# Optimization experiments

Hardware: AMD Instinct MI355X
Metric: run time of the kernel (lower is better)

## Reference

```python
import jax, jax.numpy as jnp
import numpy as np

N_NODES = 2048
N_EDGES = 32768
N_GRAPH = 64
D_INJ = 240
D_EMB = 480
D_FEAT = 512
H = 4
DH = 120
SH_DIM = 9
N_RBF = 128
CUTOFF = 5.0
AVG_DEGREE = 16.0
AVG_NUM_NODES = 32.0
N_ITER = 2
MAX_ATOM = 64


def _ln(x):
    mu = jnp.mean(x, axis=-1, keepdims=True)
    var = jnp.var(x, axis=-1, keepdims=True)
    return (x - mu) * jax.lax.rsqrt(var + 1e-6)


def _sph(u):
    # component-normalized real spherical harmonics l=0,1,2 of unit vectors u [E,3]
    x, y, z = u[:, 0], u[:, 1], u[:, 2]
    s3 = np.sqrt(3.0); s15 = np.sqrt(15.0); s5 = np.sqrt(5.0)
    return jnp.stack([
        jnp.ones_like(x),
        s3 * x, s3 * y, s3 * z,
        s15 * x * y, s15 * y * z,
        0.5 * s5 * (3.0 * z * z - 1.0),
        s15 * x * z, 0.5 * s15 * (x * x - y * y)], axis=-1)


def _block(z, esrc, edst, sh, rbf, Wq, Wk, Wv, Wsh, Wr, Wo, F1, F2, res_ffn):
    # equivariant-style dot-product attention: gather -> edge compute -> segment softmax -> scatter
    x = _ln(z)
    q = (x @ Wq)[edst].reshape(-1, H, DH)
    k = (x @ Wk)[esrc].reshape(-1, H, DH)
    v = (x @ Wv)[esrc].reshape(-1, H, DH)
    m = (sh @ Wsh).reshape(-1, H, DH)          # SH tensor-product message modulation
    r = jax.nn.silu(rbf @ Wr)[:, :, None]      # radial gate per head [E,H,1]
    k = (k + m) * r
    v = (v + m) * r
    logit = jnp.sum(q * k, axis=-1) / np.sqrt(DH)   # [E,H]
    mx = jax.ops.segment_max(logit, edst, num_segments=N_NODES)
    mx = jnp.where(jnp.isfinite(mx), mx, 0.0)
    ex = jnp.exp(logit - mx[edst])
    den = jax.ops.segment_sum(ex, edst, num_segments=N_NODES)
    alpha = ex / (den[edst] + 1e-9)
    agg = jax.ops.segment_sum(alpha[:, :, None] * v, edst, num_segments=N_NODES)
    y = z + agg.reshape(N_NODES, H * DH) @ Wo
    out = jax.nn.silu(_ln(y) @ F1) @ F2
    return y + out if res_ffn else out


def _forward(pos, atom_table, degWr, degWsh,
             b0_Wq, b0_Wk, b0_Wv, b0_Wsh, b0_Wr, b0_Wo, b0_F1, b0_F2,
             bm_Wq, bm_Wk, bm_Wv, bm_Wsh, bm_Wr, bm_Wo, bm_F1, bm_F2,
             bf_Wq, bf_Wk, bf_Wv, bf_Wsh, bf_Wr, bf_Wo, bf_F1, bf_F2,
             hW1, hW2, node_atom, edge_src, edge_dst, batch):
    # ---- encode ----
    vec = pos[edge_src] - pos[edge_dst]
    d = jnp.sqrt(jnp.sum(vec * vec, axis=-1) + 1e-12)
    sh = _sph(vec / d[:, None])                              # [E,9]
    centers = jnp.linspace(0.0, CUTOFF, N_RBF)
    width = CUTOFF / N_RBF
    rbf = jnp.exp(-0.5 * jnp.square((d[:, None] - centers) / width))  # [E,128]
    atom = atom_table[node_atom]                             # [N,240]
    rad = jax.nn.silu(rbf @ degWr)                           # [E,9]
    deg = jax.ops.segment_sum((sh * rad) @ degWsh, edge_dst, num_segments=N_NODES) / AVG_DEGREE
    inj = atom + deg                                         # input-injection features
    # ---- DEQ fixed-point (unrolled) ----
    z = jnp.zeros((N_NODES, D_EMB), dtype=pos.dtype)
    for _ in range(N_ITER):
        z = _block(jnp.concatenate([z, inj], axis=-1), edge_src, edge_dst, sh, rbf,
                   b0_Wq, b0_Wk, b0_Wv, b0_Wsh, b0_Wr, b0_Wo, b0_F1, b0_F2, False)
        for i in range(4):
            z = _block(z, edge_src, edge_dst, sh, rbf,
                       bm_Wq[i], bm_Wk[i], bm_Wv[i], bm_Wsh[i], bm_Wr[i],
                       bm_Wo[i], bm_F1[i], bm_F2[i], True)
    # ---- decode ----
    feat = _block(z, edge_src, edge_dst, sh, rbf,
                  bf_Wq, bf_Wk, bf_Wv, bf_Wsh, bf_Wr, bf_Wo, bf_F1, bf_F2, False)
    feat = _ln(feat)
    e_node = jax.nn.silu(feat @ hW1) @ hW2                   # [N,1]
    return jax.ops.segment_sum(e_node, batch, num_segments=N_GRAPH) / np.sqrt(AVG_NUM_NODES)


def setup_inputs() -> dict:
    key = jax.random.key(0)
    it = iter(jax.random.split(key, 40))
    def nrm(shape):
        fan = shape[-2] if len(shape) >= 2 else shape[-1]
        return jax.random.normal(next(it), shape, jnp.float32) / np.sqrt(fan)
    inp = {}
    inp['pos'] = jax.random.normal(next(it), (N_NODES, 3), jnp.float32) * 2.0
    inp['node_atom'] = jax.random.randint(next(it), (N_NODES,), 0, MAX_ATOM)
    inp['edge_src'] = jax.random.randint(next(it), (N_EDGES,), 0, N_NODES)
    inp['edge_dst'] = jax.random.randint(next(it), (N_EDGES,), 0, N_NODES)
    inp['batch'] = jnp.sort(jax.random.randint(next(it), (N_NODES,), 0, N_GRAPH))
    inp['atom_table'] = nrm((MAX_ATOM, D_INJ))
    inp['degWr'] = nrm((N_RBF, SH_DIM))
    inp['degWsh'] = nrm((SH_DIM, D_INJ))
    DZ = D_EMB + D_INJ
    inp['b0_Wq'] = nrm((DZ, H * DH)); inp['b0_Wk'] = nrm((DZ, H * DH)); inp['b0_Wv'] = nrm((DZ, H * DH))
    inp['b0_Wsh'] = nrm((SH_DIM, H * DH)); inp['b0_Wr'] = nrm((N_RBF, H))
    inp['b0_Wo'] = nrm((H * DH, DZ)); inp['b0_F1'] = nrm((DZ, D_EMB)); inp['b0_F2'] = nrm((D_EMB, D_EMB))
    inp['bm_Wq'] = nrm((4, D_EMB, H * DH)); inp['bm_Wk'] = nrm((4, D_EMB, H * DH)); inp['bm_Wv'] = nrm((4, D_EMB, H * DH))
    inp['bm_Wsh'] = nrm((4, SH_DIM, H * DH)); inp['bm_Wr'] = nrm((4, N_RBF, H))
    inp['bm_Wo'] = nrm((4, H * DH, D_EMB)); inp['bm_F1'] = nrm((4, D_EMB, D_EMB)); inp['bm_F2'] = nrm((4, D_EMB, D_EMB))
    inp['bf_Wq'] = nrm((D_EMB, H * DH)); inp['bf_Wk'] = nrm((D_EMB, H * DH)); inp['bf_Wv'] = nrm((D_EMB, H * DH))
    inp['bf_Wsh'] = nrm((SH_DIM, H * DH)); inp['bf_Wr'] = nrm((N_RBF, H))
    inp['bf_Wo'] = nrm((H * DH, D_EMB)); inp['bf_F1'] = nrm((D_EMB, D_EMB)); inp['bf_F2'] = nrm((D_EMB, D_FEAT))
    inp['hW1'] = nrm((D_FEAT, D_FEAT)); inp['hW2'] = nrm((D_FEAT, 1))
    return inp


def reference(pos, atom_table, degWr, degWsh,
              b0_Wq, b0_Wk, b0_Wv, b0_Wsh, b0_Wr, b0_Wo, b0_F1, b0_F2,
              bm_Wq, bm_Wk, bm_Wv, bm_Wsh, bm_Wr, bm_Wo, bm_F1, bm_F2,
              bf_Wq, bf_Wk, bf_Wv, bf_Wsh, bf_Wr, bf_Wo, bf_F1, bf_F2,
              hW1, hW2, node_atom, edge_src, edge_dst, batch):
    return _forward(pos, atom_table, degWr, degWsh,
                    b0_Wq, b0_Wk, b0_Wv, b0_Wsh, b0_Wr, b0_Wo, b0_F1, b0_F2,
                    bm_Wq, bm_Wk, bm_Wv, bm_Wsh, bm_Wr, bm_Wo, bm_F1, bm_F2,
                    bf_Wq, bf_Wk, bf_Wv, bf_Wsh, bf_Wr, bf_Wo, bf_F1, bf_F2,
                    hW1, hW2, node_atom, edge_src, edge_dst, batch)
```

## Files before the change

### kernel.cpp

```cpp
#include <hip/hip_runtime.h>

#define NN 2048
#define NE 32768
#define NG 64
#define DINJ 240
#define DEMB 480
#define DFEAT 512
#define MAXDEG 192

typedef unsigned short ushort_t;
typedef __attribute__((ext_vector_type(8))) short short8;
typedef __attribute__((ext_vector_type(4))) float floatx4;

__device__ __forceinline__ float b2f(ushort_t u){
  union { unsigned u; float f; } x; x.u = ((unsigned)u) << 16; return x.f;
}
__device__ __forceinline__ ushort_t f2b(float f){
  union { float f; unsigned u; } x; x.f = f;
  unsigned r = x.u + 0x7FFFu + ((x.u >> 16) & 1u);
  return (ushort_t)(r >> 16);
}
__device__ __forceinline__ float wredsum(float v){
  #pragma unroll
  for (int o = 32; o > 0; o >>= 1) v += __shfl_xor(v, o, 64);
  return v;
}
__device__ __forceinline__ float silu_f(float x){ return x / (1.f + __expf(-x)); }

__global__ void zero_f32(float* p, int n){
  int i = blockIdx.x*256 + threadIdx.x; if (i < n) p[i] = 0.f;
}

__global__ void detect_kernel(const ushort_t* __restrict__ probe, int* flag){
  __shared__ int c;
  if (threadIdx.x == 0) c = 0;
  __syncthreads();
  ushort_t u = probe[2*threadIdx.x];
  int e = (u >> 7) & 0xFF;
  int plausible = (u == 0) || (e >= 100 && e <= 140);
  atomicAdd(&c, plausible);
  __syncthreads();
  if (threadIdx.x == 0) *flag = (c >= 192) ? 0 : 1;
}

struct CDesc { const void* src; float* dst; int n; };
struct CDescArr { CDesc d[11]; };
__global__ __launch_bounds__(256) void convert_inputs(CDescArr ca, const int* __restrict__ flag){
  CDesc cd = ca.d[blockIdx.y];
  int isf32 = *flag;
  for (int i = blockIdx.x*256 + threadIdx.x; i < cd.n; i += gridDim.x*256){
    cd.dst[i] = isf32 ? ((const float*)cd.src)[i] : b2f(((const ushort_t*)cd.src)[i]);
  }
}

struct TDesc { const void* src; ushort_t* dh; ushort_t* dl; int K; int M; int Kpad; int Mpad; int eoff; };
struct TDescArr { TDesc d[37]; };
__global__ __launch_bounds__(256) void transpose_all(TDescArr ta, const int* __restrict__ flag){
  TDesc td = ta.d[blockIdx.z];
  int k0 = blockIdx.x*32, m0 = blockIdx.y*32;
  if (k0 >= td.Kpad || m0 >= td.Mpad) return;
  int isf32 = *flag;
  __shared__ float lds[32*33];
  int tx = threadIdx.x & 31, ty = threadIdx.x >> 5;
  #pragma unroll
  for (int r = 0; r < 4; ++r){
    int kl = ty + r*8;
    int k = k0 + kl, mm = m0 + tx;
    float x = 0.f;
    if (k < td.K && mm < td.M){
// ... 51 lines not shown
  sh[4] = s15*ix*iy; sh[5] = s15*iy*iz; sh[6] = 0.5f*s5*(3.f*iz*iz - 1.f);
  sh[7] = s15*ix*iz; sh[8] = 0.5f*s15*(ix*ix - iy*iy);
  #pragma unroll
  for (int j = 0; j < 9; ++j) sh_out[(size_t)e*9+j] = sh[j];
  float t9a[9], ga[24];
  #pragma unroll
  for (int j = 0; j < 9; ++j) t9a[j] = 0.f;
  #pragma unroll
  for (int o = 0; o < 24; ++o) ga[o] = 0.f;
  for (int k = 0; k < 128; ++k){
    float c = (float)k * (5.0f/127.0f);
    float u = (dd - c) * (128.0f/5.0f);
    float rb = __expf(-0.5f*u*u);
    const float* w9  = w9L + k*9;
    const float* w24 = w24L + k*24;
    #pragma unroll
    for (int j = 0; j < 9; ++j) t9a[j] += rb*w9[j];
    #pragma unroll
    for (int o = 0; o < 24; ++o) ga[o] += rb*w24[o];
  }
  #pragma unroll
  for (int j = 0; j < 9; ++j) t9[(size_t)e*9+j] = sh[j]*silu_f(t9a[j]);
  #pragma unroll
  for (int o = 0; o < 24; ++o){
    int slot = o >> 2, h = o & 3;
    r_all[((size_t)slot*NE + e)*4 + h] = silu_f(ga[o]);
  }
}

__global__ void hist_kernel(const int* __restrict__ edst, int* counts){
  int e = blockIdx.x*256 + threadIdx.x; if (e < NE) atomicAdd(&counts[edst[e]], 1);
}
__global__ __launch_bounds__(1024) void scan_kernel(const int* __restrict__ counts,
                                                    int* rowptr, int* cursor){
  __shared__ int s[1024];
  int t = threadIdx.x;
  int c0 = counts[2*t], c1 = counts[2*t+1];
  s[t] = c0 + c1;
  __syncthreads();
  for (int off = 1; off < 1024; off <<= 1){
    int v = (t >= off) ? s[t-off] : 0;
    __syncthreads();
    s[t] += v;
    __syncthreads();
  }
  int excl = s[t] - (c0 + c1);
  rowptr[2*t]   = excl;       cursor[2*t]   = excl;
  rowptr[2*t+1] = excl + c0;  cursor[2*t+1] = excl + c0;
  if (t == 1023) rowptr[2048] = s[1023];
}
__global__ void scatter_kernel(const int* __restrict__ edst, int* cursor, int* perm){
  int e = blockIdx.x*256 + threadIdx.x; if (e >= NE) return;
  int p = atomicAdd(&cursor[edst[e]], 1);
  perm[p] = e;
}

__global__ __launch_bounds__(64) void inj_kernel(const float* __restrict__ t9,
    const int* __restrict__ rowptr, const int* __restrict__ perm,
    const int* __restrict__ node_atom, const float* __restrict__ atom_table,
    const float* __restrict__ degWsh, float* __restrict__ inj){
  int i = blockIdx.x; int lane = threadIdx.x;
  int b = rowptr[i], e = rowptr[i+1];
  float T[9];
  #pragma unroll
  for (int j = 0; j < 9; ++j) T[j] = 0.f;
  for (int idx = b; idx < e; ++idx){
    int ed = perm[idx];
    #pragma unroll
    for (int j = 0; j < 9; ++j) T[j] += t9[(size_t)ed*9+j];
  }
  int a = node_atom[i];
  for (int c = lane; c < DINJ; c += 64){
    float s = 0.f;
    #pragma unroll
    for (int j = 0; j < 9; ++j) s += T[j]*degWsh[j*DINJ+c];
    inj[(size_t)i*DINJ+c] = atom_table[(size_t)a*DINJ+c] + s*(1.0f/16.0f);
  }
}

__global__ __launch_bounds__(256) void ln_kernel(const float* __restrict__ in, int D,
                                                 int Kpad, ushort_t* __restrict__ oh){
  int i = blockIdx.x*4 + (threadIdx.x >> 6);
  int lane = threadIdx.x & 63;
  const float* row = in + (size_t)i*D;
  float s = 0.f, sq = 0.f;
  for (int d = lane; d < D; d += 64){ float x = row[d]; s += x; sq += x*x; }
  s = wredsum(s); sq = wredsum(sq);
  float mu = s / (float)D;
  float var = fmaxf(sq / (float)D - mu*mu, 0.f);
  float rs = rsqrtf(var + 1e-6f);
  ushort_t* ohrow = oh + (size_t)i*Kpad;
  for (int d = lane; d < D; d += 64) ohrow[d] = f2b((row[d]-mu)*rs);
  for (int d = D + lane; d < Kpad; d += 64) ohrow[d] = 0;
}

__global__ __launch_bounds__(256) void ln_cat_kernel(const float* __restrict__ z,
    const float* __restrict__ inj, ushort_t* __restrict__ oh){
  int i = blockIdx.x*4 + (threadIdx.x >> 6);
  int lane = threadIdx.x & 63;
  const float* zr = z + (size_t)i*480;
  const float* ir = inj + (size_t)i*240;
  float s = 0.f, sq = 0.f;
  for (int d = lane; d < 720; d += 64){
    float x = (d < 480) ? zr[d] : ir[d-480];
    s += x; sq += x*x;
  }
  s = wredsum(s); sq = wredsum(sq);
  float mu = s * (1.0f/720.0f);
  float var = fmaxf(sq * (1.0f/720.0f) - mu*mu, 0.f);
  float rs = rsqrtf(var + 1e-6f);
  ushort_t* ohrow = oh + (size_t)i*736;
  for (int d = lane; d < 720; d += 64){
    float x = (d < 480) ? zr[d] : ir[d-480];
    ohrow[d] = f2b((x-mu)*rs);
  }
  for (int d = 720 + lane; d < 736; d += 64) ohrow[d] = 0;
}

template<int KPAD, bool SPLITB>
__global__ __launch_bounds__(256) void gemm_bt(
    const ushort_t* __restrict__ A,
    const ushort_t* __restrict__ BTh, const ushort_t* __restrict__ BTl,
    int N, int ldc,
    float* __restrict__ Cf, ushort_t* __restrict__ Cb,
    const float* __restrict__ R, const float* __restrict__ R2, int flags){
  int lane = threadIdx.x & 63, wave = threadIdx.x >> 6;
  int row0 = blockIdx.y*64 + (wave>>1)*32;
  int col0 = blockIdx.x*64 + (wave&1)*32;
  int m = lane & 15, q4 = lane >> 4;
  size_t a0 = (size_t)(row0+m)*KPAD + q4*8;
  size_t a1 = a0 + (size_t)16*KPAD;
  size_t b0 = (size_t)(col0+m)*KPAD + q4*8;
  size_t b1 = b0 + (size_t)16*KPAD;
  floatx4 acc00 = {0,0,0,0}, acc01 = {0,0,0,0}, acc10 = {0,0,0,0}, acc11 = {0,0,0,0};
  constexpr int steps = KPAD >> 5;
  constexpr int DEPTH = SPLITB ? 3 : 4;
  struct Frag { short8 A0, A1, B0h, B1h, B0l, B1l; };
  auto loadF = [&](int s) -> Frag {
    Frag f;
    size_t o = (size_t)s*32;
    f.A0  = *(const short8*)(A   + a0 + o);
    f.A1  = *(const short8*)(A   + a1 + o);
    f.B0h = *(const short8*)(BTh + b0 + o);
    f.B1h = *(const short8*)(BTh + b1 + o);
    if (SPLITB){
      f.B0l = *(const short8*)(BTl + b0 + o);
      f.B1l = *(const short8*)(BTl + b1 + o);
    }
    return f;
  };
  Frag ring[DEPTH];
  #pragma unroll
  for (int d = 0; d < DEPTH; ++d) ring[d] = loadF(d < steps ? d : steps-1);
  #pragma unroll
  for (int s = 0; s < steps; ++s){
    Frag cur = ring[s % DEPTH];
    if (s + DEPTH < steps) ring[s % DEPTH] = loadF(s + DEPTH);
    acc00 = __builtin_amdgcn_mfma_f32_16x16x32_bf16(cur.A0, cur.B0h, acc00, 0, 0, 0);
    acc01 = __builtin_amdgcn_mfma_f32_16x16x32_bf16(cur.A0, cur.B1h, acc01, 0, 0, 0);
    acc10 = __builtin_amdgcn_mfma_f32_16x16x32_bf16(cur.A1, cur.B0h, acc10, 0, 0, 0);
    acc11 = __builtin_amdgcn_mfma_f32_16x16x32_bf16(cur.A1, cur.B1h, acc11, 0, 0, 0);
    if (SPLITB){
      acc00 = __builtin_amdgcn_mfma_f32_16x16x32_bf16(cur.A0, cur.B0l, acc00, 0, 0, 0);
      acc01 = __builtin_amdgcn_mfma_f32_16x16x32_bf16(cur.A0, cur.B1l, acc01, 0, 0, 0);
      acc10 = __builtin_amdgcn_mfma_f32_16x16x32_bf16(cur.A1, cur.B0l, acc10, 0, 0, 0);
      acc11 = __builtin_amdgcn_mfma_f32_16x16x32_bf16(cur.A1, cur.B1l, acc11, 0, 0, 0);
    }
  }
  #pragma unroll
  for (int rr = 0; rr < 2; ++rr){
    #pragma unroll
    for (int cc = 0; cc < 2; ++cc){
      int col = col0 + cc*16 + m;
      if (col >= N) continue;
      floatx4 acc = rr ? (cc ? acc11 : acc10) : (cc ? acc01 : acc00);
      int rowb = row0 + rr*16 + q4*4;
      #pragma unroll
      for (int r = 0; r < 4; ++r){
        int row = rowb + r;
        float v = acc[r];
        if (flags & 16){
          if (col < 960) Cf[(size_t)row*960 + col] = v;
          else           Cb[(size_t)row*480 + (col - 960)] = f2b(v);
          continue;
        }
        size_t idx = (size_t)row*ldc + col;
        if (flags & 2){
          if (flags & 8)
            v += (col < 480) ? R[(size_t)row*480 + col] : R2[(size_t)row*240 + (col-480)];
          else
            v += R[idx];
        }
        if (flags & 1) v = silu_f(v);
        if (flags & 4) Cb[idx] = f2b(v);
        else           Cf[idx] = v;
      }
    }
  }
}

__global__ __launch_bounds__(256) void node_attn_kernel(
    const float* __restrict__ qk, const ushort_t* __restrict__ vb,
    const float* __restrict__ sh,
    const float* __restrict__ Wsh, const float* __restrict__ r_slot,
    const int* __restrict__ rowptr, const int* __restrict__ perm,
    const int* __restrict__ esrc, ushort_t* __restrict__ aggh){
  int i = blockIdx.x; int t = threadIdx.x;
  int lane = t & 63, w = t >> 6;
  int b = rowptr[i]; int deg = min(rowptr[i+1] - b, MAXDEG);
  __shared__ float qL[480];
  __shared__ float PqL[36];
  __shared__ float logitL[MAXDEG*4];
  __shared__ float rL[MAXDEG*4];
  __shared__ int eL[MAXDEG], srcL[MAXDEG];
  __shared__ float S[36];
  __shared__ float mxs[4], dens[4];
  for (int d = t; d < 480; d += 256) qL[d] = qk[(size_t)i*960 + d];
  for (int idx = t; idx < deg; idx += 256){
    int e = perm[b+idx];
    eL[idx] = e;
    srcL[idx] = esrc[e];
  }
  __syncthreads();
  if (t < 144){
    int o = t >> 2;
// ... 125 lines not shown
  const void* bm_Wsh = d_in[19];
  const void* bm_Wr  = d_in[20];
  const void* bm_Wo  = d_in[21];
  const void* bm_F1  = d_in[22];
  const void* bm_F2  = d_in[23];
  const void* bf_Wq  = d_in[24];
  const void* bf_Wk  = d_in[25];
  const void* bf_Wv  = d_in[26];
  const void* bf_Wsh = d_in[27];
  const void* bf_Wr  = d_in[28];
  const void* bf_Wo  = d_in[29];
  const void* bf_F1  = d_in[30];
  const void* bf_F2  = d_in[31];
  const void* hW1    = d_in[32];
  const void* hW2    = d_in[33];

  char* bws = (char*)d_ws;
  size_t off = 0;
  auto alloc = [&](size_t bytes) -> void* {
    void* p = bws + off;
    off += (bytes + 255) & ~(size_t)255;
    return p;
  };
  int* dflag   = (int*)alloc(256);
  float* sh_f  = (float*)alloc((size_t)NE*9*4);
  float* t9    = (float*)alloc((size_t)NE*9*4);
  int* counts  = (int*)alloc(2048*4);
  int* rowptr  = (int*)alloc(2049*4);
  int* cursor  = (int*)alloc(2048*4);
  int* perm    = (int*)alloc((size_t)NE*4);
  float* injb  = (float*)alloc((size_t)NN*DINJ*4);
  float* zA    = (float*)alloc((size_t)NN*512*4);
  float* zB    = (float*)alloc((size_t)NN*512*4);
  ushort_t* xlnh = (ushort_t*)alloc((size_t)NN*736*2);
  float* qkf   = (float*)alloc((size_t)NN*960*4);
  ushort_t* vbuf = (ushort_t*)alloc((size_t)NN*480*2);
  float* Wr_all = (float*)alloc((size_t)128*24*4);
  float* r_all = (float*)alloc((size_t)6*NE*4*4);
  ushort_t* aggh = (ushort_t*)alloc((size_t)NN*DEMB*2);
  float* ybuf  = (float*)alloc((size_t)NN*720*4);
  ushort_t* h1h = (ushort_t*)alloc((size_t)NN*DEMB*2);
  ushort_t* g1h = (ushort_t*)alloc((size_t)NN*DFEAT*2);
  float* gsum  = (float*)alloc(64*4);

  float* pos_c    = (float*)alloc((size_t)NN*3*4);
  float* atom_c   = (float*)alloc((size_t)64*DINJ*4);
  float* degWr_c  = (float*)alloc((size_t)128*9*4);
  float* degWsh_c = (float*)alloc((size_t)9*DINJ*4);
  float* b0_Wsh_c = (float*)alloc((size_t)9*480*4);
  float* b0_Wr_c  = (float*)alloc((size_t)128*4*4);
  float* bm_Wsh_c = (float*)alloc((size_t)4*9*480*4);
  float* bm_Wr_c  = (float*)alloc((size_t)4*128*4*4);
  float* bf_Wsh_c = (float*)alloc((size_t)9*480*4);
  float* bf_Wr_c  = (float*)alloc((size_t)128*4*4);
  float* hW2_c    = (float*)alloc((size_t)512*4);

  auto allocW = [&](size_t elems, ushort_t*& h, ushort_t*& l){
    h = (ushort_t*)alloc(elems*2); l = (ushort_t*)alloc(elems*2);
  };
  ushort_t *b0_qkvTh,*b0_qkvTl,*b0_WoTh,*b0_WoTl,*b0_F1Th,*b0_F1Tl,*b0_F2Th,*b0_F2Tl;
  allocW((size_t)1472*736, b0_qkvTh, b0_qkvTl);
  allocW((size_t)768*480,  b0_WoTh,  b0_WoTl);
  allocW((size_t)512*736,  b0_F1Th,  b0_F1Tl);
  allocW((size_t)512*480,  b0_F2Th,  b0_F2Tl);
  ushort_t *bm_qkvTh[4],*bm_qkvTl[4],*bm_WoTh[4],*bm_WoTl[4],*bm_F1Th[4],*bm_F1Tl[4],*bm_F2Th[4],*bm_F2Tl[4];
  for (int i = 0; i < 4; ++i){
    allocW((size_t)1472*480, bm_qkvTh[i], bm_qkvTl[i]);
    allocW((size_t)512*480,  bm_WoTh[i],  bm_WoTl[i]);
    allocW((size_t)512*480,  bm_F1Th[i],  bm_F1Tl[i]);
    allocW((size_t)512*480,  bm_F2Th[i],  bm_F2Tl[i]);
  }
  ushort_t *bf_qkvTh,*bf_qkvTl,*bf_WoTh,*bf_WoTl,*bf_F1Th,*bf_F1Tl,*bf_F2Th,*bf_F2Tl,*hW1Th,*hW1Tl;
  allocW((size_t)1472*480, bf_qkvTh, bf_qkvTl);
  allocW((size_t)512*480,  bf_WoTh,  bf_WoTl);
  allocW((size_t)512*480,  bf_F1Th,  bf_F1Tl);
  allocW((size_t)512*480,  bf_F2Th,  bf_F2Tl);
  allocW((size_t)512*512,  hW1Th,    hW1Tl);

  detect_kernel<<<1, 256, 0, stream>>>((const ushort_t*)atom_table, dflag);

  CDescArr ca;
  int ci = 0;
  auto addC = [&](const void* s, float* d, int n){
    ca.d[ci].src = s; ca.d[ci].dst = d; ca.d[ci].n = n; ++ci;
  };
  addC(pos, pos_c, NN*3);
  addC(atom_table, atom_c, 64*DINJ);
  addC(degWr, degWr_c, 128*9);
  addC(degWsh, degWsh_c, 9*DINJ);
  addC(b0_Wsh, b0_Wsh_c, 9*480);
  addC(b0_Wr, b0_Wr_c, 128*4);
  addC(bm_Wsh, bm_Wsh_c, 4*9*480);
  addC(bm_Wr, bm_Wr_c, 4*128*4);
  addC(bf_Wsh, bf_Wsh_c, 9*480);
  addC(bf_Wr, bf_Wr_c, 128*4);
  addC(hW2, hW2_c, 512);
  convert_inputs<<<dim3(8, 11), 256, 0, stream>>>(ca, dflag);

  TDescArr ta;
  int ti = 0;
  auto addT = [&](const void* s, ushort_t* dh, ushort_t* dl, int K, int M,
                  int Kp, int Mp, int rowoff, int eo){
    ta.d[ti].src = s;
    ta.d[ti].dh = dh + (size_t)rowoff*Kp;
    ta.d[ti].dl = dl + (size_t)rowoff*Kp;
    ta.d[ti].K = K; ta.d[ti].M = M; ta.d[ti].Kpad = Kp; ta.d[ti].Mpad = Mp;
    ta.d[ti].eoff = eo; ++ti;
  };
  addT(b0_Wq, b0_qkvTh, b0_qkvTl, 720, 480, 736, 480, 0,   0);
  addT(b0_Wk, b0_qkvTh, b0_qkvTl, 720, 480, 736, 480, 480, 0);
  addT(b0_Wv, b0_qkvTh, b0_qkvTl, 720, 480, 736, 512, 960, 0);
  addT(b0_Wo, b0_WoTh,  b0_WoTl,  480, 720, 480, 768, 0,   0);
  addT(b0_F1, b0_F1Th,  b0_F1Tl,  720, 480, 736, 512, 0,   0);
  addT(b0_F2, b0_F2Th,  b0_F2Tl,  480, 480, 480, 512, 0,   0);
  for (int i = 0; i < 4; ++i){
    int eo = i*480*480;
    addT(bm_Wq, bm_qkvTh[i], bm_qkvTl[i], 480, 480, 480, 480, 0,   eo);
    addT(bm_Wk, bm_qkvTh[i], bm_qkvTl[i], 480, 480, 480, 480, 480, eo);
    addT(bm_Wv, bm_qkvTh[i], bm_qkvTl[i], 480, 480, 480, 512, 960, eo);
    addT(bm_Wo, bm_WoTh[i],  bm_WoTl[i],  480, 480, 480, 512, 0,   eo);
    addT(bm_F1, bm_F1Th[i],  bm_F1Tl[i],  480, 480, 480, 512, 0,   eo);
    addT(bm_F2, bm_F2Th[i],  bm_F2Tl[i],  480, 480, 480, 512, 0,   eo);
  }
  addT(bf_Wq, bf_qkvTh, bf_qkvTl, 480, 480, 480, 480, 0,   0);
  addT(bf_Wk, bf_qkvTh, bf_qkvTl, 480, 480, 480, 480, 480, 0);
  addT(bf_Wv, bf_qkvTh, bf_qkvTl, 480, 480, 480, 512, 960, 0);
  addT(bf_Wo, bf_WoTh,  bf_WoTl,  480, 480, 480, 512, 0,   0);
  addT(bf_F1, bf_F1Th,  bf_F1Tl,  480, 480, 480, 512, 0,   0);
  addT(bf_F2, bf_F2Th,  bf_F2Tl,  480, 512, 480, 512, 0,   0);
  addT(hW1,   hW1Th,    hW1Tl,    512, 512, 512, 512, 0,   0);
  transpose_all<<<dim3(23, 24, 37), 256, 0, stream>>>(ta, dflag);

  pack_wr<<<12, 256, 0, stream>>>(b0_Wr_c, bm_Wr_c, bf_Wr_c, Wr_all);
  edge_all_kernel<<<NE/128, 128, 0, stream>>>(pos_c, esrc, edst, degWr_c, Wr_all,
                                              sh_f, t9, r_all);

  zero_f32<<<(2048 + 255)/256, 256, 0, stream>>>((float*)counts, 2048);
  hist_kernel<<<NE/256, 256, 0, stream>>>(edst, counts);
  scan_kernel<<<1, 1024, 0, stream>>>(counts, rowptr, cursor);
  scatter_kernel<<<NE/256, 256, 0, stream>>>(edst, cursor, perm);

  inj_kernel<<<NN, 64, 0, stream>>>(t9, rowptr, perm, node_atom, atom_c, degWsh_c, injb);
  zero_f32<<<(NN*DEMB)/256, 256, 0, stream>>>(zA, NN*DEMB);

  auto gemm = [&](const ushort_t* A, const ushort_t* BTh, const ushort_t* BTl,
                  int N, int Npad, int Kp, int ldc,
                  float* Cf, ushort_t* Cb, const float* R, const float* R2,
                  int flags, bool split){
    dim3 g(Npad/64, 32);
    if (split){
      if (Kp == 480)
        gemm_bt<480,true><<<g, 256, 0, stream>>>(A, BTh, BTl, N, ldc, Cf, Cb, R, R2, flags);
      else if (Kp == 512)
        gemm_bt<512,true><<<g, 256, 0, stream>>>(A, BTh, BTl, N, ldc, Cf, Cb, R, R2, flags);
      else
        gemm_bt<736,true><<<g, 256, 0, stream>>>(A, BTh, BTl, N, ldc, Cf, Cb, R, R2, flags);
    } else {
      if (Kp == 480)
        gemm_bt<480,false><<<g, 256, 0, stream>>>(A, BTh, BTl, N, ldc, Cf, Cb, R, R2, flags);
      else if (Kp == 512)
        gemm_bt<512,false><<<g, 256, 0, stream>>>(A, BTh, BTl, N, ldc, Cf, Cb, R, R2, flags);
      else
        gemm_bt<736,false><<<g, 256, 0, stream>>>(A, BTh, BTl, N, ldc, Cf, Cb, R, R2, flags);
    }
  };

  struct BW {
    const float *Wsh, *r_slot;
    const ushort_t *qkvTh,*qkvTl,*WoTh,*WoTl,*F1Th,*F1Tl,*F2Th,*F2Tl;
    int Din, Kpad, Dout; bool res;
  };
  auto run_block = [&](const BW& bw, const float* zin, const float* zinj, float* zout){
    if (zinj) ln_cat_kernel<<<NN/4, 256, 0, stream>>>(zin, zinj, xlnh);
    else      ln_kernel<<<NN/4, 256, 0, stream>>>(zin, bw.Din, bw.Kpad, xlnh);
    gemm(xlnh, bw.qkvTh, bw.qkvTl, 1440, 1472, bw.Kpad, 960,
         qkf, vbuf, nullptr, nullptr, 16, true);
    node_attn_kernel<<<NN, 256, 0, stream>>>(qkf, vbuf, sh_f, bw.Wsh, bw.r_slot,
                                             rowptr, perm, esrc, aggh);
    int WoNpad = (bw.Din == 720) ? 768 : 512;
    gemm(aggh, bw.WoTh, bw.WoTl, bw.Din, WoNpad, 480, bw.Din,
         ybuf, nullptr, zin, zinj, zinj ? (2|8) : 2, false);
    ln_kernel<<<NN/4, 256, 0, stream>>>(ybuf, bw.Din, bw.Kpad, xlnh);
    gemm(xlnh, bw.F1Th, bw.F1Tl, DEMB, 512, bw.Kpad, DEMB,
         nullptr, h1h, nullptr, nullptr, 1|4, false);
    gemm(h1h, bw.F2Th, bw.F2Tl, bw.Dout, 512, 480, bw.Dout,
         zout, nullptr, bw.res ? ybuf : nullptr, nullptr, bw.res ? 2 : 0, false);
  };

  BW b0 = { b0_Wsh_c, r_all + (size_t)0*NE*4,
            b0_qkvTh,b0_qkvTl,b0_WoTh,b0_WoTl,b0_F1Th,b0_F1Tl,b0_F2Th,b0_F2Tl,
            720, 736, 480, false };
  BW bm[4];
  for (int i = 0; i < 4; ++i){
    bm[i] = { bm_Wsh_c + (size_t)i*9*480, r_all + (size_t)(1+i)*NE*4,
              bm_qkvTh[i],bm_qkvTl[i],bm_WoTh[i],bm_WoTl[i],
              bm_F1Th[i],bm_F1Tl[i],bm_F2Th[i],bm_F2Tl[i],
              480, 480, 480, true };
  }
  BW bf = { bf_Wsh_c, r_all + (size_t)5*NE*4,
            bf_qkvTh,bf_qkvTl,bf_WoTh,bf_WoTl,bf_F1Th,bf_F1Tl,bf_F2Th,bf_F2Tl,
            480, 480, 512, false };

  float* z  = zA;
  float* z2 = zB;
  for (int iter = 0; iter < 2; ++iter){
    run_block(b0, z, injb, z2);
    { float* tmp = z; z = z2; z2 = tmp; }
    for (int i = 0; i < 4; ++i){
      run_block(bm[i], z, nullptr, z2);
      { float* tmp = z; z = z2; z2 = tmp; }
    }
  }
  run_block(bf, z, nullptr, z2);
  ln_kernel<<<NN/4, 256, 0, stream>>>(z2, DFEAT, DFEAT, xlnh);
  gemm(xlnh, hW1Th, hW1Tl, DFEAT, 512, DFEAT, DFEAT,
       nullptr, g1h, nullptr, nullptr, 1|4, true);
  zero_f32<<<1, 64, 0, stream>>>(gsum, 64);
  head_dot_kernel<<<NN/4, 256, 0, stream>>>(g1h, hW2_c, batch, gsum);
  finalize_kernel<<<1, 64, 0, stream>>>(gsum, dflag, d_out);
}
```

Measured before the change: 1.362 ms.

## Fuse LayerNorm into consumer GEMMs using row statistics from producer epilogues

Producer kernels (inj_kernel and the Wo and F2 GEMM epilogues) now write per-row partial sums and sums of squares into slot buffers. A new gemm_ln kernel adds up these partials to get each row's mean and rstd. It then normalizes and converts the fp32 A operand to bf16 as it loads it, so the standalone ln/ln_cat kernels and the bf16 xlnh buffer are gone. This cuts kernel launches and one full activation round-trip per LayerNorm. In exchange, A is read as fp32 and normalized again in every column block, most heavily in the wide QKV GEMM.

```diff
diff --git a/kernel.cpp b/kernel.cpp
--- a/kernel.cpp
+++ b/kernel.cpp
@@ -178,7 +178,8 @@
 __global__ __launch_bounds__(64) void inj_kernel(const float* __restrict__ t9,
     const int* __restrict__ rowptr, const int* __restrict__ perm,
     const int* __restrict__ node_atom, const float* __restrict__ atom_table,
-    const float* __restrict__ degWsh, float* __restrict__ inj){
+    const float* __restrict__ degWsh, float* __restrict__ inj,
+    float* __restrict__ statInj){
   int i = blockIdx.x; int lane = threadIdx.x;
   int b = rowptr[i], e = rowptr[i+1];
   float T[9];
@@ -190,51 +191,17 @@
     for (int j = 0; j < 9; ++j) T[j] += t9[(size_t)ed*9+j];
   }
   int a = node_atom[i];
+  float ss = 0.f, sq = 0.f;
   for (int c = lane; c < DINJ; c += 64){
     float s = 0.f;
     #pragma unroll
     for (int j = 0; j < 9; ++j) s += T[j]*degWsh[j*DINJ+c];
-    inj[(size_t)i*DINJ+c] = atom_table[(size_t)a*DINJ+c] + s*(1.0f/16.0f);
-  }
-}
-
-__global__ __launch_bounds__(256) void ln_kernel(const float* __restrict__ in, int D,
-                                                 int Kpad, ushort_t* __restrict__ oh){
-  int i = blockIdx.x*4 + (threadIdx.x >> 6);
-  int lane = threadIdx.x & 63;
-  const float* row = in + (size_t)i*D;
-  float s = 0.f, sq = 0.f;
-  for (int d = lane; d < D; d += 64){ float x = row[d]; s += x; sq += x*x; }
-  s = wredsum(s); sq = wredsum(sq);
-  float mu = s / (float)D;
-  float var = fmaxf(sq / (float)D - mu*mu, 0.f);
-  float rs = rsqrtf(var + 1e-6f);
-  ushort_t* ohrow = oh + (size_t)i*Kpad;
-  for (int d = lane; d < D; d += 64) ohrow[d] = f2b((row[d]-mu)*rs);
-  for (int d = D + lane; d < Kpad; d += 64) ohrow[d] = 0;
-}
-
-__global__ __launch_bounds__(256) void ln_cat_kernel(const float* __restrict__ z,
-    const float* __restrict__ inj, ushort_t* __restrict__ oh){
-  int i = blockIdx.x*4 + (threadIdx.x >> 6);
-  int lane = threadIdx.x & 63;
-  const float* zr = z + (size_t)i*480;
-  const float* ir = inj + (size_t)i*240;
-  float s = 0.f, sq = 0.f;
-  for (int d = lane; d < 720; d += 64){
-    float x = (d < 480) ? zr[d] : ir[d-480];
-    s += x; sq += x*x;
-  }
-  s = wredsum(s); sq = wredsum(sq);
-  float mu = s * (1.0f/720.0f);
-  float var = fmaxf(sq * (1.0f/720.0f) - mu*mu, 0.f);
-  float rs = rsqrtf(var + 1e-6f);
-  ushort_t* ohrow = oh + (size_t)i*736;
-  for (int d = lane; d < 720; d += 64){
-    float x = (d < 480) ? zr[d] : ir[d-480];
-    ohrow[d] = f2b((x-mu)*rs);
-  }
-  for (int d = 720 + lane; d < 736; d += 64) ohrow[d] = 0;
+    float val = atom_table[(size_t)a*DINJ+c] + s*(1.0f/16.0f);
+    inj[(size_t)i*DINJ+c] = val;
+    ss += val; sq += val*val;
+  }
+  ss = wredsum(ss); sq = wredsum(sq);
+  if (lane == 0){ statInj[i*2] = ss; statInj[i*2+1] = sq; }
 }
 
 template<int KPAD, bool SPLITB>
@@ -243,7 +210,8 @@
     const ushort_t* __restrict__ BTh, const ushort_t* __restrict__ BTl,
     int N, int ldc,
     float* __restrict__ Cf, ushort_t* __restrict__ Cb,
-    const float* __restrict__ R, const float* __restrict__ R2, int flags){
+    const float* __restrict__ R, const float* __restrict__ R2, int flags,
+    float* __restrict__ statOut){
   int lane = threadIdx.x & 63, wave = threadIdx.x >> 6;
   int row0 = blockIdx.y*64 + (wave>>1)*32;
   int col0 = blockIdx.x*64 + (wave&1)*32;
@@ -287,6 +255,153 @@
       acc11 = __builtin_amdgcn_mfma_f32_16x16x32_bf16(cur.A1, cur.B1l, acc11, 0, 0, 0);
     }
   }
+  float srow[2][4] = {{0,0,0,0},{0,0,0,0}};
+  float qrow[2][4] = {{0,0,0,0},{0,0,0,0}};
+  #pragma unroll
+  for (int rr = 0; rr < 2; ++rr){
+    #pragma unroll
+    for (int cc = 0; cc < 2; ++cc){
+      int col = col0 + cc*16 + m;
+      if (col >= N) continue;
+      floatx4 acc = rr ? (cc ? acc11 : acc10) : (cc ? acc01 : acc00);
+      int rowb = row0 + rr*16 + q4*4;
+      #pragma unroll
+      for (int r = 0; r < 4; ++r){
+        int row = rowb + r;
+        float v = acc[r];
+        size_t idx = (size_t)row*ldc + col;
+        if (flags & 2){
+          if (flags & 8)
+            v += (col < 480) ? R[(size_t)row*480 + col] : R2[(size_t)row*240 + (col-480)];
+          else
+            v += R[idx];
+        }
+        if (flags & 1) v = silu_f(v);
+        if (statOut){ srow[rr][r] += v; qrow[rr][r] += v*v; }
+        if (flags & 4) Cb[idx] = f2b(v);
+        else           Cf[idx] = v;
+      }
+    }
+  }
+  if (statOut){
+    int slot = blockIdx.x*2 + (wave&1);
+    #pragma unroll
+    for (int rr = 0; rr < 2; ++rr){
+      #pragma unroll
+      for (int r = 0; r < 4; ++r){
+        float s = srow[rr][r], q = qrow[rr][r];
+        #pragma unroll
+        for (int o = 1; o < 16; o <<= 1){
+          s += __shfl_xor(s, o, 64);
+          q += __shfl_xor(q, o, 64);
+        }
+        if (m == 0){
+          int row = row0 + rr*16 + q4*4 + r;
+          float* p = statOut + ((size_t)slot*NN + row)*2;
+          p[0] = s; p[1] = q;
+        }
+      }
+    }
+  }
+}
+
+template<int KPAD, bool SPLITB>
+__global__ __launch_bounds__(256) void gemm_ln(
+    const float* __restrict__ Az, const float* __restrict__ Ainj,
+    int L1, int L2,
+    const float* __restrict__ statA, const float* __restrict__ statInj, int nslot,
+    const ushort_t* __restrict__ BTh, const ushort_t* __restrict__ BTl,
+    int N, int ldc,
+    float* __restrict__ Cf, ushort_t* __restrict__ Cb, int flags){
+  __shared__ float muL[64], rsL[64];
+  int lane = threadIdx.x & 63, wave = threadIdx.x >> 6;
+  int row0b = blockIdx.y*64;
+  int t = threadIdx.x;
+  if (t < 64){
+    int row = row0b + t;
+    float s = 0.f, sq = 0.f;
+    for (int sl = 0; sl < nslot; ++sl){
+      const float* p = statA + ((size_t)sl*NN + row)*2;
+      s += p[0]; sq += p[1];
+    }
+    if (statInj){ s += statInj[row*2]; sq += statInj[row*2+1]; }
+    float D = (float)(L1 + L2);
+    float mu = s / D;
+    float var = fmaxf(sq / D - mu*mu, 0.f);
+    muL[t] = mu;
+    rsL[t] = rsqrtf(var + 1e-6f);
+  }
+  __syncthreads();
+  int row0 = row0b + (wave>>1)*32;
+  int col0 = blockIdx.x*64 + (wave&1)*32;
+  int m = lane & 15, q4 = lane >> 4;
+  int ra = (wave>>1)*32 + m;
+  float mu0 = muL[ra],    rs0 = rsL[ra];
+  float mu1 = muL[ra+16], rs1 = rsL[ra+16];
+  const float* pz0 = Az + (size_t)(row0 + m)*L1;
+  const float* pz1 = Az + (size_t)(row0 + 16 + m)*L1;
+  const float* pi0 = Ainj ? Ainj + (size_t)(row0 + m)*L2 : nullptr;
+  const float* pi1 = Ainj ? Ainj + (size_t)(row0 + 16 + m)*L2 : nullptr;
+  size_t b0 = (size_t)(col0+m)*KPAD + q4*8;
+  size_t b1 = b0 + (size_t)16*KPAD;
+  floatx4 acc00 = {0,0,0,0}, acc01 = {0,0,0,0}, acc10 = {0,0,0,0}, acc11 = {0,0,0,0};
+  constexpr int steps = KPAD >> 5;
+  constexpr int DEPTH = SPLITB ? 3 : 4;
+  int DD = L1 + L2;
+  auto loadA = [&](const float* pz, const float* pi, float mu, float rs, int k) -> short8 {
+    short8 r;
+    if (k + 8 <= L1){
+      float4 x0 = *(const float4*)(pz + k);
+      float4 x1 = *(const float4*)(pz + k + 4);
+      float v[8] = {x0.x,x0.y,x0.z,x0.w,x1.x,x1.y,x1.z,x1.w};
+      #pragma unroll
+      for (int j = 0; j < 8; ++j) r[j] = (short)f2b((v[j]-mu)*rs);
+    } else if (k < DD){
+      int kk = k - L1;
+      float4 x0 = *(const float4*)(pi + kk);
+      float4 x1 = *(const float4*)(pi + kk + 4);
+      float v[8] = {x0.x,x0.y,x0.z,x0.w,x1.x,x1.y,x1.z,x1.w};
+      #pragma unroll
+      for (int j = 0; j < 8; ++j) r[j] = (short)f2b((v[j]-mu)*rs);
+    } else {
+      #pragma unroll
+      for (int j = 0; j < 8; ++j) r[j] = 0;
+    }
+    return r;
+  };
+  struct Frag { short8 A0, A1, B0h, B1h, B0l, B1l; };
+  auto loadF = [&](int s) -> Frag {
+    Frag f;
+    int k = q4*8 + s*32;
+    f.A0 = loadA(pz0, pi0, mu0, rs0, k);
+    f.A1 = loadA(pz1, pi1, mu1, rs1, k);
+    size_t o = (size_t)s*32;
+    f.B0h = *(const short8*)(BTh + b0 + o);
+    f.B1h = *(const short8*)(BTh + b1 + o);
+    if (SPLITB){
+      f.B0l = *(const short8*)(BTl + b0 + o);
+      f.B1l = *(const short8*)(BTl + b1 + o);
+    }
+    return f;
+  };
+  Frag ring[DEPTH];
+  #pragma unroll
+  for (int d = 0; d < DEPTH; ++d) ring[d] = loadF(d < steps ? d : steps-1);
+  #pragma unroll
+  for (int s = 0; s < steps; ++s){
+    Frag cur = ring[s % DEPTH];
+    if (s + DEPTH < steps) ring[s % DEPTH] = loadF(s + DEPTH);
+    acc00 = __builtin_amdgcn_mfma_f32_16x16x32_bf16(cur.A0, cur.B0h, acc00, 0, 0, 0);
+    acc01 = __builtin_amdgcn_mfma_f32_16x16x32_bf16(cur.A0, cur.B1h, acc01, 0, 0, 0);
+    acc10 = __builtin_amdgcn_mfma_f32_16x16x32_bf16(cur.A1, cur.B0h, acc10, 0, 0, 0);
+    acc11 = __builtin_amdgcn_mfma_f32_16x16x32_bf16(cur.A1, cur.B1h, acc11, 0, 0, 0);
+    if (SPLITB){
+      acc00 = __builtin_amdgcn_mfma_f32_16x16x32_bf16(cur.A0, cur.B0l, acc00, 0, 0, 0);
+      acc01 = __builtin_amdgcn_mfma_f32_16x16x32_bf16(cur.A0, cur.B1l, acc01, 0, 0, 0);
+      acc10 = __builtin_amdgcn_mfma_f32_16x16x32_bf16(cur.A1, cur.B0l, acc10, 0, 0, 0);
+      acc11 = __builtin_amdgcn_mfma_f32_16x16x32_bf16(cur.A1, cur.B1l, acc11, 0, 0, 0);
+    }
+  }
   #pragma unroll
   for (int rr = 0; rr < 2; ++rr){
     #pragma unroll
@@ -305,12 +420,6 @@
           continue;
         }
         size_t idx = (size_t)row*ldc + col;
-        if (flags & 2){
-          if (flags & 8)
-            v += (col < 480) ? R[(size_t)row*480 + col] : R2[(size_t)row*240 + (col-480)];
-          else
-            v += R[idx];
-        }
         if (flags & 1) v = silu_f(v);
         if (flags & 4) Cb[idx] = f2b(v);
         else           Cf[idx] = v;
@@ -502,7 +611,6 @@
   float* injb  = (float*)alloc((size_t)NN*DINJ*4);
   float* zA    = (float*)alloc((size_t)NN*512*4);
   float* zB    = (float*)alloc((size_t)NN*512*4);
-  ushort_t* xlnh = (ushort_t*)alloc((size_t)NN*736*2);
   float* qkf   = (float*)alloc((size_t)NN*960*4);
   ushort_t* vbuf = (ushort_t*)alloc((size_t)NN*480*2);
   float* Wr_all = (float*)alloc((size_t)128*24*4);
@@ -512,6 +620,9 @@
   ushort_t* h1h = (ushort_t*)alloc((size_t)NN*DEMB*2);
   ushort_t* g1h = (ushort_t*)alloc((size_t)NN*DFEAT*2);
   float* gsum  = (float*)alloc(64*4);
+  float* statY   = (float*)alloc((size_t)24*NN*2*4);
+  float* statZ   = (float*)alloc((size_t)16*NN*2*4);
+  float* statInj = (float*)alloc((size_t)NN*2*4);
 
   float* pos_c    = (float*)alloc((size_t)NN*3*4);
   float* atom_c   = (float*)alloc((size_t)64*DINJ*4);
@@ -610,28 +721,53 @@
   scan_kernel<<<1, 1024, 0, stream>>>(counts, rowptr, cursor);
   scatter_kernel<<<NE/256, 256, 0, stream>>>(edst, cursor, perm);
 
-  inj_kernel<<<NN, 64, 0, stream>>>(t9, rowptr, perm, node_atom, atom_c, degWsh_c, injb);
+  inj_kernel<<<NN, 64, 0, stream>>>(t9, rowptr, perm, node_atom, atom_c, degWsh_c,
+                                    injb, statInj);
   zero_f32<<<(NN*DEMB)/256, 256, 0, stream>>>(zA, NN*DEMB);
+  zero_f32<<<(16*NN*2)/256, 256, 0, stream>>>(statZ, 16*NN*2);
 
   auto gemm = [&](const ushort_t* A, const ushort_t* BTh, const ushort_t* BTl,
                   int N, int Npad, int Kp, int ldc,
                   float* Cf, ushort_t* Cb, const float* R, const float* R2,
-                  int flags, bool split){
+                  int flags, bool split, float* statOut){
     dim3 g(Npad/64, 32);
     if (split){
       if (Kp == 480)
-        gemm_bt<480,true><<<g, 256, 0, stream>>>(A, BTh, BTl, N, ldc, Cf, Cb, R, R2, flags);
+        gemm_bt<480,true><<<g, 256, 0, stream>>>(A, BTh, BTl, N, ldc, Cf, Cb, R, R2, flags, statOut);
       else if (Kp == 512)
-        gemm_bt<512,true><<<g, 256, 0, stream>>>(A, BTh, BTl, N, ldc, Cf, Cb, R, R2, flags);
+        gemm_bt<512,true><<<g, 256, 0, stream>>>(A, BTh, BTl, N, ldc, Cf, Cb, R, R2, flags, statOut);
       else
-        gemm_bt<736,true><<<g, 256, 0, stream>>>(A, BTh, BTl, N, ldc, Cf, Cb, R, R2, flags);
+        gemm_bt<736,true><<<g, 256, 0, stream>>>(A, BTh, BTl, N, ldc, Cf, Cb, R, R2, flags, statOut);
     } else {
       if (Kp == 480)
-        gemm_bt<480,false><<<g, 256, 0, stream>>>(A, BTh, BTl, N, ldc, Cf, Cb, R, R2, flags);
+        gemm_bt<480,false><<<g, 256, 0, stream>>>(A, BTh, BTl, N, ldc, Cf, Cb, R, R2, flags, statOut);
       else if (Kp == 512)
-        gemm_bt<512,false><<<g, 256, 0, stream>>>(A, BTh, BTl, N, ldc, Cf, Cb, R, R2, flags);
+        gemm_bt<512,false><<<g, 256, 0, stream>>>(A, BTh, BTl, N, ldc, Cf, Cb, R, R2, flags, statOut);
       else
-        gemm_bt<736,false><<<g, 256, 0, stream>>>(A, BTh, BTl, N, ldc, Cf, Cb, R, R2, flags);
+        gemm_bt<736,false><<<g, 256, 0, stream>>>(A, BTh, BTl, N, ldc, Cf, Cb, R, R2, flags, statOut);
+    }
+  };
+
+  auto gemmLN = [&](const float* Az, const float* Ainj, int L1, int L2,
+                    const float* statA, const float* statI, int nslot,
+                    const ushort_t* BTh, const ushort_t* BTl,
+                    int N, int Npad, int Kp, int ldc,
+                    float* Cf, ushort_t* Cb, int flags, bool split){
+    dim3 g(Npad/64, 32);
+    if (split){
+      if (Kp == 480)
+        gemm_ln<480,true><<<g, 256, 0, stream>>>(Az, Ainj, L1, L2, statA, statI, nslot, BTh, BTl, N, ldc, Cf, Cb, flags);
+      else if (Kp == 512)
+        gemm_ln<512,true><<<g, 256, 0, stream>>>(Az, Ainj, L1, L2, statA, statI, nslot, BTh, BTl, N, ldc, Cf, Cb, flags);
+      else
+        gemm_ln<736,true><<<g, 256, 0, stream>>>(Az, Ainj, L1, L2, statA, statI, nslot, BTh, BTl, N, ldc, Cf, Cb, flags);
+    } else {
+      if (Kp == 480)
+        gemm_ln<480,false><<<g, 256, 0, stream>>>(Az, Ainj, L1, L2, statA, statI, nslot, BTh, BTl, N, ldc, Cf, Cb, flags);
+      else if (Kp == 512)
+        gemm_ln<512,false><<<g, 256, 0, stream>>>(Az, Ainj, L1, L2, statA, statI, nslot, BTh, BTl, N, ldc, Cf, Cb, flags);
+      else
+        gemm_ln<736,false><<<g, 256, 0, stream>>>(Az, Ainj, L1, L2, statA, statI, nslot, BTh, BTl, N, ldc, Cf, Cb, flags);
     }
   };
 
@@ -641,20 +777,17 @@
     int Din, Kpad, Dout; bool res;
   };
   auto run_block = [&](const BW& bw, const float* zin, const float* zinj, float* zout){
-    if (zinj) ln_cat_kernel<<<NN/4, 256, 0, stream>>>(zin, zinj, xlnh);
-    else      ln_kernel<<<NN/4, 256, 0, stream>>>(zin, bw.Din, bw.Kpad, xlnh);
-    gemm(xlnh, bw.qkvTh, bw.qkvTl, 1440, 1472, bw.Kpad, 960,
-         qkf, vbuf, nullptr, nullptr, 16, true);
+    gemmLN(zin, zinj, 480, zinj ? 240 : 0, statZ, zinj ? statInj : nullptr, 16,
+           bw.qkvTh, bw.qkvTl, 1440, 1472, bw.Kpad, 960, qkf, vbuf, 16, true);
     node_attn_kernel<<<NN, 256, 0, stream>>>(qkf, vbuf, sh_f, bw.Wsh, bw.r_slot,
                                              rowptr, perm, esrc, aggh);
     int WoNpad = (bw.Din == 720) ? 768 : 512;
     gemm(aggh, bw.WoTh, bw.WoTl, bw.Din, WoNpad, 480, bw.Din,
-         ybuf, nullptr, zin, zinj, zinj ? (2|8) : 2, false);
-    ln_kernel<<<NN/4, 256, 0, stream>>>(ybuf, bw.Din, bw.Kpad, xlnh);
-    gemm(xlnh, bw.F1Th, bw.F1Tl, DEMB, 512, bw.Kpad, DEMB,
-         nullptr, h1h, nullptr, nullptr, 1|4, false);
+         ybuf, nullptr, zin, zinj, zinj ? (2|8) : 2, false, statY);
+    gemmLN(ybuf, nullptr, bw.Din, 0, statY, nullptr, (WoNpad/64)*2,
+           bw.F1Th, bw.F1Tl, DEMB, 512, bw.Kpad, DEMB, nullptr, h1h, 1|4, false);
     gemm(h1h, bw.F2Th, bw.F2Tl, bw.Dout, 512, 480, bw.Dout,
-         zout, nullptr, bw.res ? ybuf : nullptr, nullptr, bw.res ? 2 : 0, false);
+         zout, nullptr, bw.res ? ybuf : nullptr, nullptr, bw.res ? 2 : 0, false, statZ);
   };
 
   BW b0 = { b0_Wsh_c, r_all + (size_t)0*NE*4,
@@ -682,9 +815,8 @@
     }
   }
   run_block(bf, z, nullptr, z2);
-  ln_kernel<<<NN/4, 256, 0, stream>>>(z2, DFEAT, DFEAT, xlnh);
-  gemm(xlnh, hW1Th, hW1Tl, DFEAT, 512, DFEAT, DFEAT,
-       nullptr, g1h, nullptr, nullptr, 1|4, true);
+  gemmLN(z2, nullptr, 512, 0, statZ, nullptr, 16,
+         hW1Th, hW1Tl, DFEAT, 512, DFEAT, DFEAT, nullptr, g1h, 1|4, true);
   zero_f32<<<1, 64, 0, stream>>>(gsum, 64);
   head_dot_kernel<<<NN/4, 256, 0, stream>>>(g1h, hW2_c, batch, gsum);
   finalize_kernel<<<1, 64, 0, stream>>>(gsum, dflag, d_out);
```

New measurement: 1.611 ms. 18.3% more time.

## Split GEMM K loop across two wave groups and fold zero-init kernels

Applied to the files above, without the earlier changes.

Adds a 512-thread GEMM variant where two groups of four waves each compute half of the K reduction for the same 64x64 tile and combine partial accumulators through shared memory before the epilogue. It is used for narrow outputs (Npad up to 768) to raise wave-level parallelism on these small GEMMs, which launch few blocks. Separately, the counts and gsum zeroing are folded into the detect and scan kernels to drop two tiny launches. The split adds an LDS round trip and a block barrier, and the partial sums are added in a different order.

```diff
diff --git a/kernel.cpp b/kernel.cpp
--- a/kernel.cpp
+++ b/kernel.cpp
@@ -31,10 +31,13 @@
   int i = blockIdx.x*256 + threadIdx.x; if (i < n) p[i] = 0.f;
 }
 
-__global__ void detect_kernel(const ushort_t* __restrict__ probe, int* flag){
+__global__ void detect_kernel(const ushort_t* __restrict__ probe, int* flag,
+                              int* __restrict__ counts){
   __shared__ int c;
   if (threadIdx.x == 0) c = 0;
   __syncthreads();
+  #pragma unroll
+  for (int r = 0; r < 8; ++r) counts[threadIdx.x*8 + r] = 0;
   ushort_t u = probe[2*threadIdx.x];
   int e = (u >> 7) & 0xFF;
   int plausible = (u == 0) || (e >= 100 && e <= 140);
@@ -152,9 +155,11 @@
   int e = blockIdx.x*256 + threadIdx.x; if (e < NE) atomicAdd(&counts[edst[e]], 1);
 }
 __global__ __launch_bounds__(1024) void scan_kernel(const int* __restrict__ counts,
-                                                    int* rowptr, int* cursor){
+                                                    int* rowptr, int* cursor,
+                                                    float* __restrict__ gsum){
   __shared__ int s[1024];
   int t = threadIdx.x;
+  if (t < 64) gsum[t] = 0.f;
   int c0 = counts[2*t], c1 = counts[2*t+1];
   s[t] = c0 + c1;
   __syncthreads();
@@ -235,6 +240,47 @@
     ohrow[d] = f2b((x-mu)*rs);
   }
   for (int d = 720 + lane; d < 736; d += 64) ohrow[d] = 0;
+}
+
+struct Frag { short8 A0, A1, B0h, B1h, B0l, B1l; };
+template<int COUNT, int BASE, bool SPLITB>
+__device__ __forceinline__ void mfma_ring(
+    const ushort_t* __restrict__ A, size_t a0, size_t a1,
+    const ushort_t* __restrict__ BTh, const ushort_t* __restrict__ BTl,
+    size_t b0, size_t b1,
+    floatx4& acc00, floatx4& acc01, floatx4& acc10, floatx4& acc11){
+  constexpr int DEPTH = SPLITB ? 3 : 4;
+  auto loadF = [&](int s) -> Frag {
+    Frag f;
+    size_t o = (size_t)(BASE + s)*32;
+    f.A0  = *(const short8*)(A   + a0 + o);
+    f.A1  = *(const short8*)(A   + a1 + o);
+    f.B0h = *(const short8*)(BTh + b0 + o);
+    f.B1h = *(const short8*)(BTh + b1 + o);
+    if (SPLITB){
+      f.B0l = *(const short8*)(BTl + b0 + o);
+      f.B1l = *(const short8*)(BTl + b1 + o);
+    }
+    return f;
+  };
+  Frag ring[DEPTH];
+  #pragma unroll
+  for (int d = 0; d < DEPTH; ++d) ring[d] = loadF(d < COUNT ? d : COUNT-1);
+  #pragma unroll
+  for (int s = 0; s < COUNT; ++s){
+    Frag cur = ring[s % DEPTH];
+    if (s + DEPTH < COUNT) ring[s % DEPTH] = loadF(s + DEPTH);
+    acc00 = __builtin_amdgcn_mfma_f32_16x16x32_bf16(cur.A0, cur.B0h, acc00, 0, 0, 0);
+    acc01 = __builtin_amdgcn_mfma_f32_16x16x32_bf16(cur.A0, cur.B1h, acc01, 0, 0, 0);
+    acc10 = __builtin_amdgcn_mfma_f32_16x16x32_bf16(cur.A1, cur.B0h, acc10, 0, 0, 0);
+    acc11 = __builtin_amdgcn_mfma_f32_16x16x32_bf16(cur.A1, cur.B1h, acc11, 0, 0, 0);
+    if (SPLITB){
+      acc00 = __builtin_amdgcn_mfma_f32_16x16x32_bf16(cur.A0, cur.B0l, acc00, 0, 0, 0);
+      acc01 = __builtin_amdgcn_mfma_f32_16x16x32_bf16(cur.A0, cur.B1l, acc01, 0, 0, 0);
+      acc10 = __builtin_amdgcn_mfma_f32_16x16x32_bf16(cur.A1, cur.B0l, acc10, 0, 0, 0);
+      acc11 = __builtin_amdgcn_mfma_f32_16x16x32_bf16(cur.A1, cur.B1l, acc11, 0, 0, 0);
+    }
+  }
 }
 
 template<int KPAD, bool SPLITB>
@@ -254,39 +300,7 @@
   size_t b1 = b0 + (size_t)16*KPAD;
   floatx4 acc00 = {0,0,0,0}, acc01 = {0,0,0,0}, acc10 = {0,0,0,0}, acc11 = {0,0,0,0};
   constexpr int steps = KPAD >> 5;
-  constexpr int DEPTH = SPLITB ? 3 : 4;
-  struct Frag { short8 A0, A1, B0h, B1h, B0l, B1l; };
-  auto loadF = [&](int s) -> Frag {
-    Frag f;
-    size_t o = (size_t)s*32;
-    f.A0  = *(const short8*)(A   + a0 + o);
-    f.A1  = *(const short8*)(A   + a1 + o);
-    f.B0h = *(const short8*)(BTh + b0 + o);
-    f.B1h = *(const short8*)(BTh + b1 + o);
-    if (SPLITB){
-      f.B0l = *(const short8*)(BTl + b0 + o);
-      f.B1l = *(const short8*)(BTl + b1 + o);
-    }
-    return f;
-  };
-  Frag ring[DEPTH];
-  #pragma unroll
-  for (int d = 0; d < DEPTH; ++d) ring[d] = loadF(d < steps ? d : steps-1);
-  #pragma unroll
-  for (int s = 0; s < steps; ++s){
-    Frag cur = ring[s % DEPTH];
-    if (s + DEPTH < steps) ring[s % DEPTH] = loadF(s + DEPTH);
-    acc00 = __builtin_amdgcn_mfma_f32_16x16x32_bf16(cur.A0, cur.B0h, acc00, 0, 0, 0);
-    acc01 = __builtin_amdgcn_mfma_f32_16x16x32_bf16(cur.A0, cur.B1h, acc01, 0, 0, 0);
-    acc10 = __builtin_amdgcn_mfma_f32_16x16x32_bf16(cur.A1, cur.B0h, acc10, 0, 0, 0);
-    acc11 = __builtin_amdgcn_mfma_f32_16x16x32_bf16(cur.A1, cur.B1h, acc11, 0, 0, 0);
-    if (SPLITB){
-      acc00 = __builtin_amdgcn_mfma_f32_16x16x32_bf16(cur.A0, cur.B0l, acc00, 0, 0, 0);
-      acc01 = __builtin_amdgcn_mfma_f32_16x16x32_bf16(cur.A0, cur.B1l, acc01, 0, 0, 0);
-      acc10 = __builtin_amdgcn_mfma_f32_16x16x32_bf16(cur.A1, cur.B0l, acc10, 0, 0, 0);
-      acc11 = __builtin_amdgcn_mfma_f32_16x16x32_bf16(cur.A1, cur.B1l, acc11, 0, 0, 0);
-    }
-  }
+  mfma_ring<steps, 0, SPLITB>(A, a0, a1, BTh, BTl, b0, b1, acc00, acc01, acc10, acc11);
   #pragma unroll
   for (int rr = 0; rr < 2; ++rr){
     #pragma unroll
@@ -304,6 +318,70 @@
           else           Cb[(size_t)row*480 + (col - 960)] = f2b(v);
           continue;
         }
+        size_t idx = (size_t)row*ldc + col;
+        if (flags & 2){
+          if (flags & 8)
+            v += (col < 480) ? R[(size_t)row*480 + col] : R2[(size_t)row*240 + (col-480)];
+          else
+            v += R[idx];
+        }
+        if (flags & 1) v = silu_f(v);
+        if (flags & 4) Cb[idx] = f2b(v);
+        else           Cf[idx] = v;
+      }
+    }
+  }
+}
+
+template<int KPAD, bool SPLITB>
+__global__ __launch_bounds__(512) void gemm_bt8(
+    const ushort_t* __restrict__ A,
+    const ushort_t* __restrict__ BTh, const ushort_t* __restrict__ BTl,
+    int N, int ldc,
+    float* __restrict__ Cf, ushort_t* __restrict__ Cb,
+    const float* __restrict__ R, const float* __restrict__ R2, int flags){
+  __shared__ float accL[4][4][256];
+  int lane = threadIdx.x & 63, wave = threadIdx.x >> 6;
+  int half = wave >> 2, w4 = wave & 3;
+  int row0 = blockIdx.y*64 + (w4>>1)*32;
+  int col0 = blockIdx.x*64 + (w4&1)*32;
+  int m = lane & 15, q4 = lane >> 4;
+  size_t a0 = (size_t)(row0+m)*KPAD + q4*8;
+  size_t a1 = a0 + (size_t)16*KPAD;
+  size_t b0 = (size_t)(col0+m)*KPAD + q4*8;
+  size_t b1 = b0 + (size_t)16*KPAD;
+  floatx4 acc00 = {0,0,0,0}, acc01 = {0,0,0,0}, acc10 = {0,0,0,0}, acc11 = {0,0,0,0};
+  constexpr int steps = KPAD >> 5;
+  constexpr int S0 = (steps + 1) >> 1;
+  constexpr int S1 = steps - S0;
+  if (half == 0)
+    mfma_ring<S0, 0,  SPLITB>(A, a0, a1, BTh, BTl, b0, b1, acc00, acc01, acc10, acc11);
+  else
+    mfma_ring<S1, S0, SPLITB>(A, a0, a1, BTh, BTl, b0, b1, acc00, acc01, acc10, acc11);
+  if (half == 1){
+    *(floatx4*)&accL[w4][0][lane*4] = acc00;
+    *(floatx4*)&accL[w4][1][lane*4] = acc01;
+    *(floatx4*)&accL[w4][2][lane*4] = acc10;
+    *(floatx4*)&accL[w4][3][lane*4] = acc11;
+  }
+  __syncthreads();
+  if (half == 1) return;
+  acc00 += *(const floatx4*)&accL[w4][0][lane*4];
+  acc01 += *(const floatx4*)&accL[w4][1][lane*4];
+  acc10 += *(const floatx4*)&accL[w4][2][lane*4];
+  acc11 += *(const floatx4*)&accL[w4][3][lane*4];
+  #pragma unroll
+  for (int rr = 0; rr < 2; ++rr){
+    #pragma unroll
+    for (int cc = 0; cc < 2; ++cc){
+      int col = col0 + cc*16 + m;
+      if (col >= N) continue;
+      floatx4 acc = rr ? (cc ? acc11 : acc10) : (cc ? acc01 : acc00);
+      int rowb = row0 + rr*16 + q4*4;
+      #pragma unroll
+      for (int r = 0; r < 4; ++r){
+        int row = rowb + r;
+        float v = acc[r];
         size_t idx = (size_t)row*ldc + col;
         if (flags & 2){
           if (flags & 8)
@@ -547,7 +625,7 @@
   allocW((size_t)512*480,  bf_F2Th,  bf_F2Tl);
   allocW((size_t)512*512,  hW1Th,    hW1Tl);
 
-  detect_kernel<<<1, 256, 0, stream>>>((const ushort_t*)atom_table, dflag);
+  detect_kernel<<<1, 256, 0, stream>>>((const ushort_t*)atom_table, dflag, counts);
 
   CDescArr ca;
   int ci = 0;
@@ -605,9 +683,8 @@
   edge_all_kernel<<<NE/128, 128, 0, stream>>>(pos_c, esrc, edst, degWr_c, Wr_all,
                                               sh_f, t9, r_all);
 
-  zero_f32<<<(2048 + 255)/256, 256, 0, stream>>>((float*)counts, 2048);
   hist_kernel<<<NE/256, 256, 0, stream>>>(edst, counts);
-  scan_kernel<<<1, 1024, 0, stream>>>(counts, rowptr, cursor);
+  scan_kernel<<<1, 1024, 0, stream>>>(counts, rowptr, cursor, gsum);
   scatter_kernel<<<NE/256, 256, 0, stream>>>(edst, cursor, perm);
 
   inj_kernel<<<NN, 64, 0, stream>>>(t9, rowptr, perm, node_atom, atom_c, degWsh_c, injb);
@@ -618,6 +695,24 @@
                   float* Cf, ushort_t* Cb, const float* R, const float* R2,
                   int flags, bool split){
     dim3 g(Npad/64, 32);
+    if (Npad <= 768){
+      if (split){
+        if (Kp == 480)
+          gemm_bt8<480,true><<<g, 512, 0, stream>>>(A, BTh, BTl, N, ldc, Cf, Cb, R, R2, flags);
+        else if (Kp == 512)
+          gemm_bt8<512,true><<<g, 512, 0, stream>>>(A, BTh, BTl, N, ldc, Cf, Cb, R, R2, flags);
+        else
+          gemm_bt8<736,true><<<g, 512, 0, stream>>>(A, BTh, BTl, N, ldc, Cf, Cb, R, R2, flags);
+      } else {
+        if (Kp == 480)
+          gemm_bt8<480,false><<<g, 512, 0, stream>>>(A, BTh, BTl, N, ldc, Cf, Cb, R, R2, flags);
+        else if (Kp == 512)
+          gemm_bt8<512,false><<<g, 512, 0, stream>>>(A, BTh, BTl, N, ldc, Cf, Cb, R, R2, flags);
+        else
+          gemm_bt8<736,false><<<g, 512, 0, stream>>>(A, BTh, BTl, N, ldc, Cf, Cb, R, R2, flags);
+      }
+      return;
+    }
     if (split){
       if (Kp == 480)
         gemm_bt<480,true><<<g, 256, 0, stream>>>(A, BTh, BTl, N, ldc, Cf, Cb, R, R2, flags);
@@ -685,7 +780,6 @@
   ln_kernel<<<NN/4, 256, 0, stream>>>(z2, DFEAT, DFEAT, xlnh);
   gemm(xlnh, hW1Th, hW1Tl, DFEAT, 512, DFEAT, DFEAT,
        nullptr, g1h, nullptr, nullptr, 1|4, true);
-  zero_f32<<<1, 64, 0, stream>>>(gsum, 64);
   head_dot_kernel<<<NN/4, 256, 0, stream>>>(g1h, hW2_c, batch, gsum);
   finalize_kernel<<<1, 64, 0, stream>>>(gsum, dflag, d_out);
 }
```

Result: no change. 1.358 ms (-0.3%).
